# Kernel tuning notes

Hardware: AMD Instinct MI355X
Metric: run time of the kernel (lower is better)

The kernel has to match this reference:

```python
import jax, jax.numpy as jnp
import numpy as np

B, S, D = 8, 4096, 1024
E, R, K = 6, 16, 2


def setup_inputs() -> dict:
    key = jax.random.key(0)
    ks = jax.random.split(key, 9)
    sc = 0.02
    return {
        "x": jax.random.normal(ks[0], (B, S, D), jnp.float32),
        "base_W": jax.random.normal(ks[1], (D, D), jnp.float32) * sc,
        "base_b": jax.random.normal(ks[2], (D,), jnp.float32) * sc,
        "shared_A": jax.random.normal(ks[3], (R, D), jnp.float32) * sc,
        "shared_B": jax.random.normal(ks[4], (D, R), jnp.float32) * sc,
        "routed_A": jax.random.normal(ks[5], (E, R, D), jnp.float32) * sc,
        "routed_B": jax.random.normal(ks[6], (E, D, R), jnp.float32) * sc,
        "router_W": jax.random.normal(ks[7], (E, D), jnp.float32) * sc,
        "router_b": jax.random.normal(ks[8], (E,), jnp.float32) * sc,
    }


def reference(x, base_W, base_b, shared_A, shared_B, routed_A, routed_B, router_W, router_b):
    # Frozen base linear (torch.no_grad in the original)
    base_out = jax.lax.stop_gradient(jnp.einsum("bsi,oi->bso", x, base_W) + base_b)

    # Shared expert (num_shared = 1): low-rank in->rank->out
    shared_out = jnp.einsum("bsr,or->bso", jnp.einsum("bsi,ri->bsr", x, shared_A), shared_B)

    # Router: softmax over experts, top-k, scatter back to sparse weights, renormalize
    logits = jnp.einsum("bsi,ei->bse", x, router_W) + router_b
    gate = jax.nn.softmax(logits, axis=-1)                      # [B,S,E]
    topk_w, topk_i = jax.lax.top_k(gate, K)                     # [B,S,K]
    sparse_w = jnp.sum(jax.nn.one_hot(topk_i, E, dtype=gate.dtype) * topk_w[..., None], axis=-2)  # [B,S,E]
    sparse_w = sparse_w / (jnp.sum(sparse_w, axis=-1, keepdims=True) + 1e-6)

    # Dense compute of all routed experts (faithful to the torch.stack), then weighted combine
    h = jnp.einsum("bsi,eri->bser", x, routed_A)                # [B,S,E,R]
    routed_outs = jnp.einsum("bser,eor->bseo", h, routed_B)     # [B,S,E,out]
    routed_out = jnp.einsum("bseo,bse->bso", routed_outs, sparse_w)

    return base_out + shared_out + routed_out
```

## Files before the change

kernel.cpp:

```cpp
#include <hip/hip_runtime.h>
#include <hip/hip_bf16.h>

typedef unsigned short u16;
typedef __attribute__((ext_vector_type(8))) __bf16 bf16x8;
typedef __attribute__((ext_vector_type(4))) float f32x4;

#define NTOK 32768
#define XLDA 1152
#define WS_XU  0
#define WS_WSP 75497472
#define WS_WP  76546048
#define WS_W1T 78905344

static __device__ __forceinline__ u16 f2bf(float f) {
  __hip_bfloat16 h = __float2bfloat16(f);
  return __builtin_bit_cast(u16, h);
}

#define GLOAD_LDS16(g, l)                                                     \
  __builtin_amdgcn_global_load_lds(                                           \
      (const __attribute__((address_space(1))) void*)(g),                     \
      (__attribute__((address_space(3))) void*)(l), 16, 0, 0)

__global__ __launch_bounds__(256) void pack_weights(
    const float* __restrict__ baseW, const float* __restrict__ sharedA,
    const float* __restrict__ sharedB, const float* __restrict__ routedA,
    const float* __restrict__ routedB, u16* __restrict__ Wp, u16* __restrict__ W1t) {
  int idx = blockIdx.x * 256 + threadIdx.x;
  const int NWP = 1024 * 1152;
  if (idx < NWP) {
    int o = idx / 1152, k = idx - o * 1152;
    float v;
    if (k < 1024)      v = baseW[o * 1024 + k];
    else if (k < 1040) v = sharedB[o * 16 + (k - 1024)];
    else if (k < 1136) { int c = k - 1040; v = routedB[((c >> 4) * 1024 + o) * 16 + (c & 15)]; }
    else               v = 0.0f;
    Wp[idx] = f2bf(v);
  } else {
    int j = idx - NWP;
    int n = j >> 10, k = j & 1023;
    float v;
    if (n < 16)       v = sharedA[n * 1024 + k];
    else if (n < 112) v = routedA[(n - 16) * 1024 + k];
    else              v = 0.0f;
    W1t[j] = f2bf(v);
  }
}

__global__ __launch_bounds__(256) void convert_router(
    const float* __restrict__ x, const float* __restrict__ rW, const float* __restrict__ rB,
    u16* __restrict__ xu, float* __restrict__ wsp) {
  int tid = threadIdx.x, lane = tid & 63, wid = tid >> 6;
  int wg = blockIdx.x * 4 + wid;
  float4 rw[6][4];
  #pragma unroll
  for (int e = 0; e < 6; ++e)
    #pragma unroll
    for (int c = 0; c < 4; ++c)
      rw[e][c] = *(const float4*)&rW[e * 1024 + c * 256 + lane * 4];
  float rbias[6];
  #pragma unroll
  for (int e = 0; e < 6; ++e) rbias[e] = rB[e];

  for (int ti = 0; ti < 4; ++ti) {
    int t = wg * 4 + ti;
    float4 xv[4];
    #pragma unroll
    for (int c = 0; c < 4; ++c) xv[c] = *(const float4*)&x[t * 1024 + c * 256 + lane * 4];
    #pragma unroll
    for (int c = 0; c < 4; ++c) {
      ushort4 o;
      o.x = f2bf(xv[c].x); o.y = f2bf(xv[c].y); o.z = f2bf(xv[c].z); o.w = f2bf(xv[c].w);
      *(ushort4*)&xu[t * XLDA + c * 256 + lane * 4] = o;
    }
    float lg[6];
    #pragma unroll
    for (int e = 0; e < 6; ++e) {
      float s = 0.f;
      #pragma unroll
      for (int c = 0; c < 4; ++c)
        s += xv[c].x * rw[e][c].x + xv[c].y * rw[e][c].y +
             xv[c].z * rw[e][c].z + xv[c].w * rw[e][c].w;
      #pragma unroll
      for (int off = 32; off > 0; off >>= 1) s += __shfl_xor(s, off);
      lg[e] = s + rbias[e];
    }
    float mx = lg[0];
    #pragma unroll
    for (int e = 1; e < 6; ++e) mx = fmaxf(mx, lg[e]);
    float ex[6], ssum = 0.f;
    #pragma unroll
    for (int e = 0; e < 6; ++e) { ex[e] = __expf(lg[e] - mx); ssum += ex[e]; }
    float inv = 1.0f / ssum;
    int i1 = 0; float v1 = ex[0];
    #pragma unroll
    for (int e = 1; e < 6; ++e) if (ex[e] > v1) { v1 = ex[e]; i1 = e; }
    int i2 = -1; float v2 = -1.0f;
    #pragma unroll
    for (int e = 0; e < 6; ++e) if (e != i1 && ex[e] > v2) { v2 = ex[e]; i2 = e; }
    float g1 = v1 * inv, g2 = v2 * inv;
    float den = g1 + g2 + 1e-6f;
    if (lane < 6) {
      float wv = (lane == i1) ? g1 / den : ((lane == i2) ? g2 / den : 0.0f);
      wsp[t * 8 + lane] = wv;
    }
  }
}

__global__ __launch_bounds__(256) void gemm_small(
    const u16* __restrict__ A, int lda, const u16* __restrict__ B, int ldb, int ktiles,
    u16* __restrict__ uout, const float* __restrict__ wsp) {
  __shared__ u16 As[128 * 64];
  __shared__ u16 Bs[128 * 64];
  int tid = threadIdx.x, lane = tid & 63, wid = tid >> 6;
  int wr = wid >> 1, wc = wid & 1;
  int rowbase = blockIdx.x * 128, colbase = 0;

  f32x4 acc[4][4];
  #pragma unroll
  for (int m = 0; m < 4; ++m)
    #pragma unroll
    for (int n = 0; n < 4; ++n) acc[m][n] = f32x4{0.f, 0.f, 0.f, 0.f};

  int srow = (lane >> 3);
  int scol = (lane & 7) * 8;

  for (int kt = 0; kt < ktiles; ++kt) {
    __syncthreads();
    #pragma unroll
    for (int i = 0; i < 4; ++i) {
      int j = wid * 4 + i;
      int row = j * 8 + srow;
      GLOAD_LDS16(A + (size_t)(rowbase + row) * lda + kt * 64 + scol, As + j * 512);
      GLOAD_LDS16(B + (size_t)(colbase + row) * ldb + kt * 64 + scol, Bs + j * 512);
    }
    __syncthreads();
    #pragma unroll
    for (int ks = 0; ks < 2; ++ks) {
      bf16x8 af[4], bfv[4];
      #pragma unroll
      for (int m = 0; m < 4; ++m)
        af[m] = *(const bf16x8*)&As[(wr * 64 + m * 16 + (lane & 15)) * 64 + ks * 32 + (lane >> 4) * 8];
      #pragma unroll
      for (int n = 0; n < 4; ++n)
        bfv[n] = *(const bf16x8*)&Bs[(wc * 64 + n * 16 + (lane & 15)) * 64 + ks * 32 + (lane >> 4) * 8];
      #pragma unroll
      for (int m = 0; m < 4; ++m)
        #pragma unroll
        for (int n = 0; n < 4; ++n)
          acc[m][n] = __builtin_amdgcn_mfma_f32_16x16x32_bf16(af[m], bfv[n], acc[m][n], 0, 0, 0);
    }
  }

  int row0 = rowbase + wr * 64 + ((lane >> 4) << 2);
  int col0 = colbase + wc * 64 + (lane & 15);
  #pragma unroll
  for (int n = 0; n < 4; ++n) {
    int col = col0 + n * 16;
    int e = (col - 16) >> 4;
    #pragma unroll
    for (int m = 0; m < 4; ++m) {
      int rbase = row0 + m * 16;
      #pragma unroll
      for (int r = 0; r < 4; ++r) {
        int t = rbase + r;
        float f = (col < 16) ? 1.0f : ((col < 112) ? wsp[t * 8 + e] : 0.0f);
        uout[(size_t)t * XLDA + 1024 + col] = f2bf(acc[m][n][r] * f);
      }
    }
  }
}

#define KT_TOTAL 18

#define VMW()  asm volatile("s_waitcnt vmcnt(4)" ::: "memory")
#define VMW0() asm volatile("s_waitcnt vmcnt(0)" ::: "memory")
#define LGW()  asm volatile("s_waitcnt lgkmcnt(0)" ::: "memory")
#define BAR()  __builtin_amdgcn_s_barrier()

__global__ __launch_bounds__(512, 2) void gemm256(
    const u16* __restrict__ A, const u16* __restrict__ B,
    float* __restrict__ out, const float* __restrict__ bias) {
  extern __shared__ char lds[];
  const int lda = XLDA, ldb = XLDA;
  const int tid = threadIdx.x, lane = tid & 63, wid = tid >> 6;
  const int wr = wid >> 2, wcn = wid & 3;

  int bid = blockIdx.x;
  int xcd = bid & 7, idx = bid >> 3;
  int bx = xcd * 16 + (idx >> 2);
  int by = idx & 3;
  const int rowbase = bx * 256, colbase = by * 256;

  f32x4 acc[8][4];
  #pragma unroll
  for (int m = 0; m < 8; ++m)
    #pragma unroll
    for (int n = 0; n < 4; ++n) acc[m][n] = f32x4{0.f, 0.f, 0.f, 0.f};

  const int l3 = lane >> 3, l7 = lane & 7;
  const int kperm = ((l7 ^ l3) << 3);
  const u16* aSrc = A + (size_t)(rowbase + wr * 128 + wcn * 16 + l3) * lda + kperm;
  const int aDst = (wr * 128 + wcn * 16) * 128;
  const int bh = wcn >> 1, bq = wcn & 1;
  const u16* bSrc = B + (size_t)(colbase + bh * 128 + wr * 64 + bq * 16 + l3) * ldb + kperm;
  const int bDst = (bh * 128 + wr * 64 + bq * 16) * 128;

#define STAGE_A(bufp, kt, g) do {                                   \
    const u16* _s = aSrc + (g) * 64 * lda + (kt) * 64;              \
    char* _d = lds + (bufp) * 65536 + aDst + (g) * 64 * 128;        \
    GLOAD_LDS16(_s, _d);                                            \
    GLOAD_LDS16(_s + 8 * lda, _d + 8 * 128);                        \
  } while (0)
#define STAGE_B(bufp, kt, g) do {                                   \
    const u16* _s = bSrc + (g) * 32 * ldb + (kt) * 64;              \
    char* _d = lds + (bufp) * 65536 + 32768 + bDst + (g) * 32 * 128;\
    GLOAD_LDS16(_s, _d);                                            \
    GLOAD_LDS16(_s + 8 * ldb, _d + 8 * 128);                        \
  } while (0)

  const int fr = lane & 15, fq = lane >> 4;
  const int sswz = (lane & 7) << 4;

  auto LDA_ = [&](int bufp, int mh, bf16x8* a) {
    const char* base = lds + bufp * 65536 + (wr * 128 + mh * 64 + fr) * 128;
    #pragma unroll
    for (int m = 0; m < 4; ++m)
      #pragma unroll
      for (int ks = 0; ks < 2; ++ks)
        a[m * 2 + ks] = *(const bf16x8*)(base + m * 16 * 128 + ((ks * 64 + fq * 16) ^ sswz));
  };
  auto LDB_ = [&](int bufp, int nh, bf16x8* b) {
    const char* base = lds + bufp * 65536 + 32768 + (wcn * 64 + nh * 32 + fr) * 128;
    #pragma unroll
    for (int n = 0; n < 2; ++n)
      #pragma unroll
      for (int ks = 0; ks < 2; ++ks)
        b[n * 2 + ks] = *(const bf16x8*)(base + n * 16 * 128 + ((ks * 64 + fq * 16) ^ sswz));
  };
  auto MF = [&](bf16x8* a, bf16x8* b, int mo, int no) {
    __builtin_amdgcn_s_setprio(1);
    #pragma unroll
    for (int m = 0; m < 4; ++m)
      #pragma unroll
      for (int n = 0; n < 2; ++n)
        #pragma unroll
        for (int ks = 0; ks < 2; ++ks)
          acc[mo + m][no + n] = __builtin_amdgcn_mfma_f32_16x16x32_bf16(
              a[m * 2 + ks], b[n * 2 + ks], acc[mo + m][no + n], 0, 0, 0);
    __builtin_amdgcn_s_setprio(0);
  };

  STAGE_A(0, 0, 0); STAGE_B(0, 0, 0); STAGE_B(0, 0, 1); STAGE_A(0, 0, 1);
  VMW0(); BAR();

  bf16x8 a[8], b0[4], b1[4];
  for (int t = 0; t < 9; ++t) {
    LDA_(0, 0, a); LDB_(0, 0, b0);
    STAGE_A(1, 2 * t + 1, 0);
    VMW(); BAR(); LGW();
    MF(a, b0, 0, 0); BAR();

    LDB_(0, 1, b1);
    STAGE_B(1, 2 * t + 1, 0);
    VMW(); BAR(); LGW();
    MF(a, b1, 0, 2); BAR();

    LDA_(0, 1, a);
    STAGE_B(1, 2 * t + 1, 1);
    VMW(); BAR(); LGW();
    MF(a, b1, 4, 2); BAR();

    STAGE_A(1, 2 * t + 1, 1);
    VMW(); BAR();
    MF(a, b0, 4, 0); BAR();

    LDA_(1, 0, a); LDB_(1, 0, b0);
    if (t < 8) STAGE_A(0, 2 * t + 2, 0);
    VMW(); BAR(); LGW();
    MF(a, b0, 0, 0); BAR();

    LDB_(1, 1, b1);
    if (t < 8) STAGE_B(0, 2 * t + 2, 0);
    VMW(); BAR(); LGW();
    MF(a, b1, 0, 2); BAR();

    LDA_(1, 1, a);
    if (t < 8) STAGE_B(0, 2 * t + 2, 1);
    VMW(); BAR(); LGW();
    MF(a, b1, 4, 2); BAR();

    if (t < 8) STAGE_A(0, 2 * t + 2, 1);
    VMW(); BAR();
    MF(a, b0, 4, 0); BAR();
  }

  int row0 = rowbase + wr * 128 + (fq << 2);
  int col0 = colbase + wcn * 64 + fr;
  #pragma unroll
  for (int n = 0; n < 4; ++n) {
    int col = col0 + n * 16;
    float bv = bias[col];
    #pragma unroll
    for (int m = 0; m < 8; ++m) {
      int rb = row0 + m * 16;
      #pragma unroll
      for (int r = 0; r < 4; ++r)
        out[(size_t)(rb + r) * 1024 + col] = acc[m][n][r] + bv;
    }
  }
#undef STAGE_A
#undef STAGE_B
}

extern "C" void kernel_launch(void* const* d_in, const int* in_sizes, int n_in,
                              void* d_out, int out_size, void* d_ws, size_t ws_size,
                              hipStream_t stream) {
  const float* x       = (const float*)d_in[0];
  const float* baseW   = (const float*)d_in[1];
  const float* baseb   = (const float*)d_in[2];
  const float* sharedA = (const float*)d_in[3];
  const float* sharedB = (const float*)d_in[4];
  const float* routedA = (const float*)d_in[5];
  const float* routedB = (const float*)d_in[6];
  const float* routerW = (const float*)d_in[7];
  const float* routerb = (const float*)d_in[8];
  float* out = (float*)d_out;
  char* ws = (char*)d_ws;
  u16*   xu  = (u16*)(ws + WS_XU);
  float* wsp = (float*)(ws + WS_WSP);
  u16*   Wp  = (u16*)(ws + WS_WP);
  u16*   W1t = (u16*)(ws + WS_W1T);

  static int lds_attr_set = 0;
  if (!lds_attr_set) {
    hipFuncSetAttribute((const void*)gemm256,
                        hipFuncAttributeMaxDynamicSharedMemorySize, 131072);
    lds_attr_set = 1;
  }

  pack_weights<<<5120, 256, 0, stream>>>(baseW, sharedA, sharedB, routedA, routedB, Wp, W1t);
  convert_router<<<2048, 256, 0, stream>>>(x, routerW, routerb, xu, wsp);
  gemm_small<<<dim3(256, 1), 256, 0, stream>>>(xu, XLDA, W1t, 1024, 16, xu, wsp);
  gemm256<<<dim3(512, 1), 512, 131072, stream>>>(xu, Wp, out, baseb);
}
```

Baseline: 163.2 us.

## Fuse x conversion, router softmax/top-k, and low-rank GEMM into one kernel

Merges the convert_router and gemm_small kernels into a single expert_fused kernel. Each block loads fp32 x tiles, converts them to bf16 in LDS and in the workspace, accumulates router logits from an LDS copy of router_W, and computes the gate weights in shared memory before the epilogue. This removes one launch, the reread of bf16 x from global memory, and the wsp round trip. The cost is only 256 blocks doing the fp32 conversion, with synchronous x loads that are not pipelined against the MFMA loop, so per-block latency may rise.

```diff
diff --git a/kernel.cpp b/kernel.cpp
--- a/kernel.cpp
+++ b/kernel.cpp
@@ -3,14 +3,14 @@
 
 typedef unsigned short u16;
 typedef __attribute__((ext_vector_type(8))) __bf16 bf16x8;
+typedef __attribute__((ext_vector_type(8))) unsigned short u16x8;
 typedef __attribute__((ext_vector_type(4))) float f32x4;
 
 #define NTOK 32768
 #define XLDA 1152
 #define WS_XU  0
-#define WS_WSP 75497472
-#define WS_WP  76546048
-#define WS_W1T 78905344
+#define WS_WP  75497472
+#define WS_W1T 77856768
 
 static __device__ __forceinline__ u16 f2bf(float f) {
   __hip_bfloat16 h = __float2bfloat16(f);
@@ -47,92 +47,71 @@
   }
 }
 
-__global__ __launch_bounds__(256) void convert_router(
+__global__ __launch_bounds__(256) void expert_fused(
     const float* __restrict__ x, const float* __restrict__ rW, const float* __restrict__ rB,
-    u16* __restrict__ xu, float* __restrict__ wsp) {
-  int tid = threadIdx.x, lane = tid & 63, wid = tid >> 6;
-  int wg = blockIdx.x * 4 + wid;
-  float4 rw[6][4];
-  #pragma unroll
-  for (int e = 0; e < 6; ++e)
-    #pragma unroll
-    for (int c = 0; c < 4; ++c)
-      rw[e][c] = *(const float4*)&rW[e * 1024 + c * 256 + lane * 4];
-  float rbias[6];
-  #pragma unroll
-  for (int e = 0; e < 6; ++e) rbias[e] = rB[e];
-
-  for (int ti = 0; ti < 4; ++ti) {
-    int t = wg * 4 + ti;
-    float4 xv[4];
-    #pragma unroll
-    for (int c = 0; c < 4; ++c) xv[c] = *(const float4*)&x[t * 1024 + c * 256 + lane * 4];
-    #pragma unroll
-    for (int c = 0; c < 4; ++c) {
-      ushort4 o;
-      o.x = f2bf(xv[c].x); o.y = f2bf(xv[c].y); o.z = f2bf(xv[c].z); o.w = f2bf(xv[c].w);
-      *(ushort4*)&xu[t * XLDA + c * 256 + lane * 4] = o;
-    }
-    float lg[6];
-    #pragma unroll
-    for (int e = 0; e < 6; ++e) {
-      float s = 0.f;
-      #pragma unroll
-      for (int c = 0; c < 4; ++c)
-        s += xv[c].x * rw[e][c].x + xv[c].y * rw[e][c].y +
-             xv[c].z * rw[e][c].z + xv[c].w * rw[e][c].w;
-      #pragma unroll
-      for (int off = 32; off > 0; off >>= 1) s += __shfl_xor(s, off);
-      lg[e] = s + rbias[e];
-    }
-    float mx = lg[0];
-    #pragma unroll
-    for (int e = 1; e < 6; ++e) mx = fmaxf(mx, lg[e]);
-    float ex[6], ssum = 0.f;
-    #pragma unroll
-    for (int e = 0; e < 6; ++e) { ex[e] = __expf(lg[e] - mx); ssum += ex[e]; }
-    float inv = 1.0f / ssum;
-    int i1 = 0; float v1 = ex[0];
-    #pragma unroll
-    for (int e = 1; e < 6; ++e) if (ex[e] > v1) { v1 = ex[e]; i1 = e; }
-    int i2 = -1; float v2 = -1.0f;
-    #pragma unroll
-    for (int e = 0; e < 6; ++e) if (e != i1 && ex[e] > v2) { v2 = ex[e]; i2 = e; }
-    float g1 = v1 * inv, g2 = v2 * inv;
-    float den = g1 + g2 + 1e-6f;
-    if (lane < 6) {
-      float wv = (lane == i1) ? g1 / den : ((lane == i2) ? g2 / den : 0.0f);
-      wsp[t * 8 + lane] = wv;
-    }
-  }
-}
-
-__global__ __launch_bounds__(256) void gemm_small(
-    const u16* __restrict__ A, int lda, const u16* __restrict__ B, int ldb, int ktiles,
-    u16* __restrict__ uout, const float* __restrict__ wsp) {
+    const u16* __restrict__ W1t, u16* __restrict__ xu) {
+  __shared__ float rWs[6 * 1024];
   __shared__ u16 As[128 * 64];
   __shared__ u16 Bs[128 * 64];
-  int tid = threadIdx.x, lane = tid & 63, wid = tid >> 6;
-  int wr = wid >> 1, wc = wid & 1;
-  int rowbase = blockIdx.x * 128, colbase = 0;
-
+  __shared__ float wspS[128][8];
+  const int tid = threadIdx.x, lane = tid & 63, wid = tid >> 6;
+  const int T0 = blockIdx.x * 128;
+
+  for (int i = tid; i < 1536; i += 256)
+    ((float4*)rWs)[i] = ((const float4*)rW)[i];
+
+  float lp[4][6];
+  #pragma unroll
+  for (int i = 0; i < 4; ++i)
+    #pragma unroll
+    for (int e = 0; e < 6; ++e) lp[i][e] = 0.f;
   f32x4 acc[4][4];
   #pragma unroll
   for (int m = 0; m < 4; ++m)
     #pragma unroll
     for (int n = 0; n < 4; ++n) acc[m][n] = f32x4{0.f, 0.f, 0.f, 0.f};
 
-  int srow = (lane >> 3);
-  int scol = (lane & 7) * 8;
-
-  for (int kt = 0; kt < ktiles; ++kt) {
+  const int rloc = tid >> 3;
+  const int kc = tid & 7;
+  const int srow = lane >> 3, scol = (lane & 7) * 8;
+  const int wr = wid >> 1, wc = wid & 1;
+
+  for (int kt = 0; kt < 16; ++kt) {
     __syncthreads();
     #pragma unroll
     for (int i = 0; i < 4; ++i) {
       int j = wid * 4 + i;
-      int row = j * 8 + srow;
-      GLOAD_LDS16(A + (size_t)(rowbase + row) * lda + kt * 64 + scol, As + j * 512);
-      GLOAD_LDS16(B + (size_t)(colbase + row) * ldb + kt * 64 + scol, Bs + j * 512);
+      GLOAD_LDS16(W1t + (size_t)(j * 8 + srow) * 1024 + kt * 64 + scol, Bs + j * 512);
+    }
+    float4 v[4][2];
+    #pragma unroll
+    for (int i = 0; i < 4; ++i) {
+      int r = i * 32 + rloc;
+      const float4* p = (const float4*)(x + (size_t)(T0 + r) * 1024 + kt * 64 + kc * 8);
+      v[i][0] = p[0]; v[i][1] = p[1];
+    }
+    #pragma unroll
+    for (int i = 0; i < 4; ++i) {
+      int r = i * 32 + rloc;
+      u16x8 o;
+      o[0] = f2bf(v[i][0].x); o[1] = f2bf(v[i][0].y);
+      o[2] = f2bf(v[i][0].z); o[3] = f2bf(v[i][0].w);
+      o[4] = f2bf(v[i][1].x); o[5] = f2bf(v[i][1].y);
+      o[6] = f2bf(v[i][1].z); o[7] = f2bf(v[i][1].w);
+      *(u16x8*)&As[r * 64 + kc * 8] = o;
+      *(u16x8*)&xu[(size_t)(T0 + r) * XLDA + kt * 64 + kc * 8] = o;
+    }
+    {
+      int kb = kt * 64 + kc * 8;
+      #pragma unroll
+      for (int e = 0; e < 6; ++e) {
+        float4 w0 = *(const float4*)&rWs[e * 1024 + kb];
+        float4 w1 = *(const float4*)&rWs[e * 1024 + kb + 4];
+        #pragma unroll
+        for (int i = 0; i < 4; ++i)
+          lp[i][e] += v[i][0].x * w0.x + v[i][0].y * w0.y + v[i][0].z * w0.z + v[i][0].w * w0.w
+                    + v[i][1].x * w1.x + v[i][1].y * w1.y + v[i][1].z * w1.z + v[i][1].w * w1.w;
+      }
     }
     __syncthreads();
     #pragma unroll
@@ -152,26 +131,60 @@
     }
   }
 
-  int row0 = rowbase + wr * 64 + ((lane >> 4) << 2);
-  int col0 = colbase + wc * 64 + (lane & 15);
+  #pragma unroll
+  for (int m = 1; m <= 4; m <<= 1)
+    #pragma unroll
+    for (int i = 0; i < 4; ++i)
+      #pragma unroll
+      for (int e = 0; e < 6; ++e)
+        lp[i][e] += __shfl_xor(lp[i][e], m);
+
+  if ((lane & 7) == 0) {
+    #pragma unroll
+    for (int i = 0; i < 4; ++i) {
+      int r = i * 32 + rloc;
+      float lg[6];
+      #pragma unroll
+      for (int e = 0; e < 6; ++e) lg[e] = lp[i][e] + rB[e];
+      float mx = lg[0];
+      #pragma unroll
+      for (int e = 1; e < 6; ++e) mx = fmaxf(mx, lg[e]);
+      float ex[6], ssum = 0.f;
+      #pragma unroll
+      for (int e = 0; e < 6; ++e) { ex[e] = __expf(lg[e] - mx); ssum += ex[e]; }
+      float inv = 1.0f / ssum;
+      int i1 = 0; float v1 = ex[0];
+      #pragma unroll
+      for (int e = 1; e < 6; ++e) if (ex[e] > v1) { v1 = ex[e]; i1 = e; }
+      int i2 = -1; float v2 = -1.0f;
+      #pragma unroll
+      for (int e = 0; e < 6; ++e) if (e != i1 && ex[e] > v2) { v2 = ex[e]; i2 = e; }
+      float g1 = v1 * inv, g2 = v2 * inv;
+      float den = g1 + g2 + 1e-6f;
+      #pragma unroll
+      for (int e = 0; e < 6; ++e)
+        wspS[r][e] = (e == i1) ? g1 / den : ((e == i2) ? g2 / den : 0.0f);
+    }
+  }
+  __syncthreads();
+
+  int row0 = wr * 64 + ((lane >> 4) << 2);
+  int col0 = wc * 64 + (lane & 15);
   #pragma unroll
   for (int n = 0; n < 4; ++n) {
     int col = col0 + n * 16;
     int e = (col - 16) >> 4;
     #pragma unroll
     for (int m = 0; m < 4; ++m) {
-      int rbase = row0 + m * 16;
       #pragma unroll
       for (int r = 0; r < 4; ++r) {
-        int t = rbase + r;
-        float f = (col < 16) ? 1.0f : ((col < 112) ? wsp[t * 8 + e] : 0.0f);
-        uout[(size_t)t * XLDA + 1024 + col] = f2bf(acc[m][n][r] * f);
+        int rl = row0 + m * 16 + r;
+        float f = (col < 16) ? 1.0f : ((col < 112) ? wspS[rl][e] : 0.0f);
+        xu[(size_t)(T0 + rl) * XLDA + 1024 + col] = f2bf(acc[m][n][r] * f);
       }
     }
   }
 }
-
-#define KT_TOTAL 18
 
 #define VMW()  asm volatile("s_waitcnt vmcnt(4)" ::: "memory")
 #define VMW0() asm volatile("s_waitcnt vmcnt(0)" ::: "memory")
@@ -327,20 +340,14 @@
   const float* routerb = (const float*)d_in[8];
   float* out = (float*)d_out;
   char* ws = (char*)d_ws;
-  u16*   xu  = (u16*)(ws + WS_XU);
-  float* wsp = (float*)(ws + WS_WSP);
-  u16*   Wp  = (u16*)(ws + WS_WP);
-  u16*   W1t = (u16*)(ws + WS_W1T);
-
-  static int lds_attr_set = 0;
-  if (!lds_attr_set) {
-    hipFuncSetAttribute((const void*)gemm256,
-                        hipFuncAttributeMaxDynamicSharedMemorySize, 131072);
-    lds_attr_set = 1;
-  }
+  u16* xu  = (u16*)(ws + WS_XU);
+  u16* Wp  = (u16*)(ws + WS_WP);
+  u16* W1t = (u16*)(ws + WS_W1T);
+
+  hipFuncSetAttribute((const void*)gemm256,
+                      hipFuncAttributeMaxDynamicSharedMemorySize, 131072);
 
   pack_weights<<<5120, 256, 0, stream>>>(baseW, sharedA, sharedB, routedA, routedB, Wp, W1t);
-  convert_router<<<2048, 256, 0, stream>>>(x, routerW, routerb, xu, wsp);
-  gemm_small<<<dim3(256, 1), 256, 0, stream>>>(xu, XLDA, W1t, 1024, 16, xu, wsp);
+  expert_fused<<<256, 256, 0, stream>>>(x, routerW, routerb, W1t, xu);
   gemm256<<<dim3(512, 1), 512, 131072, stream>>>(xu, Wp, out, baseb);
 }
```

After: 155.2 us. 4.9% less time.
